# Kernel optimization log

Hardware: AMD Instinct MI355X
Metric: run time of the kernel (lower is better)

Reference implementation:

```python
import jax, jax.numpy as jnp
import numpy as np

S = 4096
DMODEL = 1024
DK = 128

def setup_inputs() -> dict:
    key = jax.random.key(0)
    ks = jax.random.split(key, 7)
    X = jax.random.normal(ks[0], (S, DMODEL), dtype=jnp.float32)
    # nn.Linear(dmodel, dk): weight [dk, dmodel], bias [dk]
    sc = 1.0 / np.sqrt(DMODEL)
    Wq = jax.random.uniform(ks[1], (DK, DMODEL), jnp.float32, -sc, sc)
    bq = jax.random.uniform(ks[2], (DK,), jnp.float32, -sc, sc)
    Wk = jax.random.uniform(ks[3], (DK, DMODEL), jnp.float32, -sc, sc)
    bk = jax.random.uniform(ks[4], (DK,), jnp.float32, -sc, sc)
    Wv = jax.random.uniform(ks[5], (DK, DMODEL), jnp.float32, -sc, sc)
    bv = jax.random.uniform(ks[6], (DK,), jnp.float32, -sc, sc)
    return {"X": X, "Wq": Wq, "bq": bq, "Wk": Wk, "bk": bk, "Wv": Wv, "bv": bv}

def reference(X, Wq, bq, Wk, bk, Wv, bv):
    # QKV projections: [S, dk]
    Q = X @ Wq.T + bq
    K = X @ Wk.T + bk
    V = X @ Wv.T + bv
    scale = 1.0 / jnp.sqrt(jnp.asarray(DK, X.dtype))
    scores = (Q @ K.T) * scale  # [S, S]
    s = X.shape[0]
    causal = jnp.tril(jnp.ones((s, s), dtype=bool))  # True = keep
    scores = jnp.where(causal, scores, -jnp.inf)
    A = jax.nn.softmax(scores, axis=-1)  # dropout p=0 -> identity
    return A @ V  # [S, dk]
```

## Files before the change

kernel.cpp:

```cpp
#include <hip/hip_runtime.h>
#include <hip/hip_bf16.h>

#define S 4096
#define DMODEL 1024
#define DK 128

typedef __attribute__((ext_vector_type(8))) short  short8;
typedef __attribute__((ext_vector_type(4))) float  f32x4;

__device__ __forceinline__ unsigned short f2bf(float f) {
    return __builtin_bit_cast(unsigned short, __float2bfloat16(f));
}

__device__ __forceinline__ short8 cvt8(float4 a, float4 b) {
    short8 v;
    v[0] = (short)f2bf(a.x); v[1] = (short)f2bf(a.y);
    v[2] = (short)f2bf(a.z); v[3] = (short)f2bf(a.w);
    v[4] = (short)f2bf(b.x); v[5] = (short)f2bf(b.y);
    v[6] = (short)f2bf(b.z); v[7] = (short)f2bf(b.w);
    return v;
}

__global__ __launch_bounds__(256) void cvt_kernel(
    const float* __restrict__ X,
    const float* __restrict__ Wq, const float* __restrict__ Wk,
    const float* __restrict__ Wv,
    unsigned short* __restrict__ Xb, unsigned short* __restrict__ Wb)
{
    const int i = blockIdx.x * 256 + threadIdx.x;
    const float* __restrict__ src;
    unsigned short* __restrict__ dst;
    size_t off;
    if (i < 524288) {
        src = X; dst = Xb; off = (size_t)i * 8;
    } else {
        const int j   = i - 524288;
        const int sel = j >> 14, jj = j & 16383;
        src = sel == 0 ? Wq : sel == 1 ? Wk : Wv;
        dst = Wb + (size_t)sel * DK * DMODEL;
        off = (size_t)jj * 8;
    }
    const float4 a = *(const float4*)(src + off);
    const float4 b = *(const float4*)(src + off + 4);
    *(short8*)(dst + off) = cvt8(a, b);
}

__global__ __launch_bounds__(256) void proj_gemm(
    const unsigned short* __restrict__ Xb, const unsigned short* __restrict__ Wb,
    const float* __restrict__ bq, const float* __restrict__ bk,
    const float* __restrict__ bv,
    unsigned short* __restrict__ Qb, unsigned short* __restrict__ Kb,
    unsigned short* __restrict__ Vb)
{
    const int sel = blockIdx.y;
    const float* __restrict__ bias = sel == 0 ? bq : sel == 1 ? bk : bv;
    unsigned short* __restrict__ Out = sel == 0 ? Qb : sel == 1 ? Kb : Vb;
    const unsigned short* __restrict__ wbase = Wb + (size_t)sel * DK * DMODEL;

    const int tid = threadIdx.x, w = tid >> 6, lane = tid & 63;
    const int li = lane & 15, gl = lane >> 4;
    const int r0 = blockIdx.x * 16;
    const int n0 = w * 32;

    f32x4 acc[2];
    #pragma unroll
    for (int j = 0; j < 2; ++j)
        #pragma unroll
        for (int r = 0; r < 4; ++r) acc[j][r] = 0.f;

    const unsigned short* ap = &Xb[(size_t)(r0 + li) * DMODEL + 8 * gl];
    const unsigned short* bp0 = &wbase[(size_t)(n0 + li) * DMODEL + 8 * gl];
    const unsigned short* bp1 = &wbase[(size_t)(n0 + 16 + li) * DMODEL + 8 * gl];

    #pragma unroll 4
    for (int k0 = 0; k0 < DMODEL; k0 += 32) {
        const short8 a  = *(const short8*)(ap + k0);
        const short8 b0 = *(const short8*)(bp0 + k0);
        const short8 b1 = *(const short8*)(bp1 + k0);
        acc[0] = __builtin_amdgcn_mfma_f32_16x16x32_bf16(a, b0, acc[0], 0, 0, 0);
        acc[1] = __builtin_amdgcn_mfma_f32_16x16x32_bf16(a, b1, acc[1], 0, 0, 0);
    }

    #pragma unroll
    for (int j = 0; j < 2; ++j)
        #pragma unroll
        for (int r = 0; r < 4; ++r) {
            const int row = r0 + 4 * gl + r;
            const int col = n0 + 16 * j + li;
            Out[(size_t)row * DK + col] = f2bf(acc[j][r] + bias[col]);
        }
}

__global__ __launch_bounds__(256) void transpose_v(
    const unsigned short* __restrict__ Vb, unsigned short* __restrict__ Vt)
{
    __shared__ unsigned short tile[64][72];
    const int s0 = blockIdx.x * 64, d0 = blockIdx.y * 64;
    const int t = threadIdx.x;
    const int r = t >> 2, cc = (t & 3) * 16;

    const short8* src = (const short8*)&Vb[(size_t)(s0 + r) * DK + d0 + cc];
    const short8 a = src[0], b = src[1];
    #pragma unroll
    for (int i = 0; i < 8; ++i) {
        tile[r][cc + i]     = (unsigned short)a[i];
        tile[r][cc + 8 + i] = (unsigned short)b[i];
    }
    __syncthreads();

    short8 o0, o1;
    #pragma unroll
    for (int i = 0; i < 8; ++i) {
        o0[i] = (short)tile[cc + i][r];
        o1[i] = (short)tile[cc + 8 + i][r];
    }
    short8* dst = (short8*)&Vt[(size_t)(d0 + r) * S + s0 + cc];
    dst[0] = o0; dst[1] = o1;
}

__global__ __launch_bounds__(64) void attn_mfma(
    const unsigned short* __restrict__ Qb,
    const unsigned short* __restrict__ Kb,
    const unsigned short* __restrict__ Vt,
    float* __restrict__ OP, float* __restrict__ ML)
{
    const int b = blockIdx.x;
    int g;
    if      (b <  32) g = 0; else if (b <  96) g = 1;
    else if (b < 192) g = 2; else if (b < 320) g = 3;
    else if (b < 480) g = 4; else if (b < 672) g = 5;
    else if (b < 896) g = 6; else               g = 7;
    const int off = b - 16 * g * (g + 1);
    const int qt  = 32 * g + off / (g + 1);
    const int c   = off % (g + 1);
    const int kstart = c * 512;
    const int kend   = min((c + 1) * 512, 16 * qt + 16);

    const int lane = threadIdx.x, li = lane & 15, gl = lane >> 4;
    const int qrow = 16 * qt + li;

    __shared__ unsigned short Pl[16][40];

    short8 aq[4];
    #pragma unroll
    for (int s = 0; s < 4; ++s)
        aq[s] = *(const short8*)&Qb[(size_t)qrow * DK + 32 * s + 8 * gl];

    f32x4 accv[8];
    #pragma unroll
    for (int n = 0; n < 8; ++n)
        #pragma unroll
        for (int r = 0; r < 4; ++r) accv[n][r] = 0.f;

    float mrow[4] = {-1e30f, -1e30f, -1e30f, -1e30f};
    float lrow[4] = {0.f, 0.f, 0.f, 0.f};
    const float scale = 0.08838834764831845f;

    for (int kb = kstart; kb < kend; kb += 32) {
        short8 bk[2][4], bv[8];
        #pragma unroll
        for (int kt = 0; kt < 2; ++kt)
            #pragma unroll
            for (int s = 0; s < 4; ++s)
                bk[kt][s] = *(const short8*)
                    &Kb[(size_t)(kb + 16 * kt + li) * DK + 32 * s + 8 * gl];
        #pragma unroll
        for (int n = 0; n < 8; ++n)
            bv[n] = *(const short8*)&Vt[(size_t)(16 * n + li) * S + kb + 8 * gl];

        f32x4 sc[2];
        #pragma unroll
        for (int kt = 0; kt < 2; ++kt)
            #pragma unroll
            for (int r = 0; r < 4; ++r) sc[kt][r] = 0.f;
        #pragma unroll
        for (int kt = 0; kt < 2; ++kt)
            #pragma unroll
            for (int s = 0; s < 4; ++s)
                sc[kt] = __builtin_amdgcn_mfma_f32_16x16x32_bf16(
                    aq[s], bk[kt][s], sc[kt], 0, 0, 0);

        float p[2][4];
        #pragma unroll
        for (int kt = 0; kt < 2; ++kt)
            #pragma unroll
            for (int r = 0; r < 4; ++r) {
                const int key = kb + 16 * kt + li;
                const int q   = 16 * qt + 4 * gl + r;
                p[kt][r] = (key > q) ? -1e30f : sc[kt][r] * scale;
            }

        #pragma unroll
        for (int r = 0; r < 4; ++r) {
            float t = fmaxf(p[0][r], p[1][r]);
            t = fmaxf(t, __shfl_xor(t, 1));
            t = fmaxf(t, __shfl_xor(t, 2));
            t = fmaxf(t, __shfl_xor(t, 4));
            t = fmaxf(t, __shfl_xor(t, 8));
            const float mnew = fmaxf(mrow[r], t);
            const float corr = __expf(mrow[r] - mnew);
            p[0][r] = __expf(p[0][r] - mnew);
            p[1][r] = __expf(p[1][r] - mnew);
            float ps = p[0][r] + p[1][r];
            ps += __shfl_xor(ps, 1);
            ps += __shfl_xor(ps, 2);
            ps += __shfl_xor(ps, 4);
            ps += __shfl_xor(ps, 8);
            lrow[r] = lrow[r] * corr + ps;
            mrow[r] = mnew;
            #pragma unroll
            for (int n = 0; n < 8; ++n) accv[n][r] *= corr;
        }

        #pragma unroll
        for (int kt = 0; kt < 2; ++kt)
            #pragma unroll
            for (int r = 0; r < 4; ++r)
                Pl[4 * gl + r][16 * kt + li] = f2bf(p[kt][r]);
        __syncthreads();
        const short8 pa = *(const short8*)&Pl[li][8 * gl];
        __syncthreads();

        #pragma unroll
        for (int n = 0; n < 8; ++n)
            accv[n] = __builtin_amdgcn_mfma_f32_16x16x32_bf16(pa, bv[n], accv[n], 0, 0, 0);
    }

    #pragma unroll
    for (int n = 0; n < 8; ++n)
        #pragma unroll
        for (int r = 0; r < 4; ++r)
            OP[((size_t)b * 16 + 4 * gl + r) * DK + 16 * n + li] = accv[n][r];
    if (li == 0) {
        #pragma unroll
        for (int r = 0; r < 4; ++r) {
            ML[((size_t)b * 16 + 4 * gl + r) * 2 + 0] = mrow[r];
            ML[((size_t)b * 16 + 4 * gl + r) * 2 + 1] = lrow[r];
        }
    }
}

__global__ __launch_bounds__(DK) void merge_kernel(
    const float* __restrict__ OP, const float* __restrict__ ML,
    float* __restrict__ out)
{
    const int row = blockIdx.x, dv = threadIdx.x;
    const int qt = row >> 4, ql = row & 15;
    const int g  = qt >> 5;
    const int base = 16 * g * (g + 1) + (qt & 31) * (g + 1);

    float M = -1e30f;
    for (int c = 0; c <= g; ++c)
        M = fmaxf(M, ML[((size_t)(base + c) * 16 + ql) * 2]);
    float L = 0.f, o = 0.f;
    for (int c = 0; c <= g; ++c) {
        const float mc = ML[((size_t)(base + c) * 16 + ql) * 2 + 0];
        const float lc = ML[((size_t)(base + c) * 16 + ql) * 2 + 1];
        const float wgt = __expf(mc - M);
        L += lc * wgt;
        o += wgt * OP[((size_t)(base + c) * 16 + ql) * DK + dv];
    }
    out[(size_t)row * DK + dv] = o / L;
}

extern "C" void kernel_launch(void* const* d_in, const int* in_sizes, int n_in,
                              void* d_out, int out_size, void* d_ws, size_t ws_size,
                              hipStream_t stream)
{
    (void)in_sizes; (void)n_in; (void)out_size; (void)ws_size;
    const float* X  = (const float*)d_in[0];
    const float* Wq = (const float*)d_in[1];
    const float* bq = (const float*)d_in[2];
    const float* Wk = (const float*)d_in[3];
    const float* bk = (const float*)d_in[4];
    const float* Wv = (const float*)d_in[5];
    const float* bv = (const float*)d_in[6];
    float* out = (float*)d_out;

    unsigned short* Wb = (unsigned short*)d_ws;
    unsigned short* Qb = Wb + (size_t)3 * DK * DMODEL;
    unsigned short* Kb = Qb + (size_t)S * DK;
    unsigned short* Vb = Kb + (size_t)S * DK;
    unsigned short* Vt = Vb + (size_t)S * DK;
    unsigned short* Xb = Vt + (size_t)S * DK;
    float* OP = (float*)Xb;
    float* ML = OP + (size_t)1152 * 16 * DK;

    cvt_kernel<<<2240, 256, 0, stream>>>(X, Wq, Wk, Wv, Xb, Wb);
    proj_gemm<<<dim3(S / 16, 3), 256, 0, stream>>>(
        Xb, Wb, bq, bk, bv, Qb, Kb, Vb);
    transpose_v<<<dim3(S / 64, DK / 64), 256, 0, stream>>>(Vb, Vt);
    attn_mfma<<<1152, 64, 0, stream>>>(Qb, Kb, Vt, OP, ML);
    merge_kernel<<<S, DK, 0, stream>>>(OP, ML, out);
}
```

Baseline: 159.6 us.

## Enlarge attention query tile to 32 rows, prefetch K, add lazy rescale

The attention kernel now processes 32 query rows per wavefront, sharing each loaded K/V tile across two 16-row subtiles. It also uses 256-key chunks with a new split schedule of 1088 blocks, software-prefetches the next K tile, and skips the online-softmax rescale unless the running max grows by more than a threshold. MFMA sections are bracketed with s_setprio. The projection GEMM uses 2 waves each computing 64 output columns instead of 4 waves of 32, so each A fragment is reused across more MFMAs. The cost is more registers per wave and fewer blocks, with some risk of lower occupancy. The lazy rescale leans on exp values staying bounded when the max shifts by less than the threshold.

```diff
diff --git a/kernel.cpp b/kernel.cpp
--- a/kernel.cpp
+++ b/kernel.cpp
@@ -45,7 +45,7 @@
     *(short8*)(dst + off) = cvt8(a, b);
 }
 
-__global__ __launch_bounds__(256) void proj_gemm(
+__global__ __launch_bounds__(128) void proj_gemm(
     const unsigned short* __restrict__ Xb, const unsigned short* __restrict__ Wb,
     const float* __restrict__ bq, const float* __restrict__ bk,
     const float* __restrict__ bv,
@@ -60,29 +60,35 @@
     const int tid = threadIdx.x, w = tid >> 6, lane = tid & 63;
     const int li = lane & 15, gl = lane >> 4;
     const int r0 = blockIdx.x * 16;
-    const int n0 = w * 32;
-
-    f32x4 acc[2];
-    #pragma unroll
-    for (int j = 0; j < 2; ++j)
+    const int n0 = w * 64;
+
+    f32x4 acc[4];
+    #pragma unroll
+    for (int j = 0; j < 4; ++j)
         #pragma unroll
         for (int r = 0; r < 4; ++r) acc[j][r] = 0.f;
 
     const unsigned short* ap = &Xb[(size_t)(r0 + li) * DMODEL + 8 * gl];
     const unsigned short* bp0 = &wbase[(size_t)(n0 + li) * DMODEL + 8 * gl];
-    const unsigned short* bp1 = &wbase[(size_t)(n0 + 16 + li) * DMODEL + 8 * gl];
+    const unsigned short* bp1 = bp0 + (size_t)16 * DMODEL;
+    const unsigned short* bp2 = bp0 + (size_t)32 * DMODEL;
+    const unsigned short* bp3 = bp0 + (size_t)48 * DMODEL;
 
     #pragma unroll 4
     for (int k0 = 0; k0 < DMODEL; k0 += 32) {
         const short8 a  = *(const short8*)(ap + k0);
         const short8 b0 = *(const short8*)(bp0 + k0);
         const short8 b1 = *(const short8*)(bp1 + k0);
+        const short8 b2 = *(const short8*)(bp2 + k0);
+        const short8 b3 = *(const short8*)(bp3 + k0);
         acc[0] = __builtin_amdgcn_mfma_f32_16x16x32_bf16(a, b0, acc[0], 0, 0, 0);
         acc[1] = __builtin_amdgcn_mfma_f32_16x16x32_bf16(a, b1, acc[1], 0, 0, 0);
-    }
-
-    #pragma unroll
-    for (int j = 0; j < 2; ++j)
+        acc[2] = __builtin_amdgcn_mfma_f32_16x16x32_bf16(a, b2, acc[2], 0, 0, 0);
+        acc[3] = __builtin_amdgcn_mfma_f32_16x16x32_bf16(a, b3, acc[3], 0, 0, 0);
+    }
+
+    #pragma unroll
+    for (int j = 0; j < 4; ++j)
         #pragma unroll
         for (int r = 0; r < 4; ++r) {
             const int row = r0 + 4 * gl + r;
@@ -125,118 +131,183 @@
     float* __restrict__ OP, float* __restrict__ ML)
 {
     const int b = blockIdx.x;
-    int g;
-    if      (b <  32) g = 0; else if (b <  96) g = 1;
-    else if (b < 192) g = 2; else if (b < 320) g = 3;
-    else if (b < 480) g = 4; else if (b < 672) g = 5;
-    else if (b < 896) g = 6; else               g = 7;
-    const int off = b - 16 * g * (g + 1);
-    const int qt  = 32 * g + off / (g + 1);
+    int g = 0;
+    while (4 * (g + 1) * (g + 2) <= b) ++g;
+    const int off = b - 4 * g * (g + 1);
+    const int t   = 8 * g + off / (g + 1);
     const int c   = off % (g + 1);
-    const int kstart = c * 512;
-    const int kend   = min((c + 1) * 512, 16 * qt + 16);
+    const int kstart = c * 256;
+    const int kend   = min((c + 1) * 256, 32 * t + 32);
 
     const int lane = threadIdx.x, li = lane & 15, gl = lane >> 4;
-    const int qrow = 16 * qt + li;
-
-    __shared__ unsigned short Pl[16][40];
-
-    short8 aq[4];
-    #pragma unroll
-    for (int s = 0; s < 4; ++s)
-        aq[s] = *(const short8*)&Qb[(size_t)qrow * DK + 32 * s + 8 * gl];
-
-    f32x4 accv[8];
-    #pragma unroll
-    for (int n = 0; n < 8; ++n)
-        #pragma unroll
-        for (int r = 0; r < 4; ++r) accv[n][r] = 0.f;
-
-    float mrow[4] = {-1e30f, -1e30f, -1e30f, -1e30f};
-    float lrow[4] = {0.f, 0.f, 0.f, 0.f};
+
+    __shared__ unsigned short Pl[32][40];
+
+    short8 aq[2][4];
+    #pragma unroll
+    for (int qs = 0; qs < 2; ++qs)
+        #pragma unroll
+        for (int s = 0; s < 4; ++s)
+            aq[qs][s] = *(const short8*)
+                &Qb[(size_t)(32 * t + 16 * qs + li) * DK + 32 * s + 8 * gl];
+
+    f32x4 accv[2][8];
+    #pragma unroll
+    for (int qs = 0; qs < 2; ++qs)
+        #pragma unroll
+        for (int n = 0; n < 8; ++n)
+            #pragma unroll
+            for (int r = 0; r < 4; ++r) accv[qs][n][r] = 0.f;
+
+    float mrow[2][4], lrow[2][4];
+    #pragma unroll
+    for (int qs = 0; qs < 2; ++qs)
+        #pragma unroll
+        for (int r = 0; r < 4; ++r) { mrow[qs][r] = -1e30f; lrow[qs][r] = 0.f; }
+
     const float scale = 0.08838834764831845f;
 
+    short8 bkc[2][4], bkn[2][4];
+    #pragma unroll
+    for (int kt = 0; kt < 2; ++kt)
+        #pragma unroll
+        for (int s = 0; s < 4; ++s)
+            bkc[kt][s] = *(const short8*)
+                &Kb[(size_t)(kstart + 16 * kt + li) * DK + 32 * s + 8 * gl];
+
     for (int kb = kstart; kb < kend; kb += 32) {
-        short8 bk[2][4], bv[8];
-        #pragma unroll
-        for (int kt = 0; kt < 2; ++kt)
-            #pragma unroll
-            for (int s = 0; s < 4; ++s)
-                bk[kt][s] = *(const short8*)
-                    &Kb[(size_t)(kb + 16 * kt + li) * DK + 32 * s + 8 * gl];
+        short8 bv[8];
         #pragma unroll
         for (int n = 0; n < 8; ++n)
             bv[n] = *(const short8*)&Vt[(size_t)(16 * n + li) * S + kb + 8 * gl];
 
-        f32x4 sc[2];
+        f32x4 sc[2][2];
+        #pragma unroll
+        for (int qs = 0; qs < 2; ++qs)
+            #pragma unroll
+            for (int kt = 0; kt < 2; ++kt)
+                #pragma unroll
+                for (int r = 0; r < 4; ++r) sc[qs][kt][r] = 0.f;
+        __builtin_amdgcn_s_setprio(1);
+        #pragma unroll
+        for (int qs = 0; qs < 2; ++qs)
+            #pragma unroll
+            for (int kt = 0; kt < 2; ++kt)
+                #pragma unroll
+                for (int s = 0; s < 4; ++s)
+                    sc[qs][kt] = __builtin_amdgcn_mfma_f32_16x16x32_bf16(
+                        aq[qs][s], bkc[kt][s], sc[qs][kt], 0, 0, 0);
+        __builtin_amdgcn_s_setprio(0);
+
+        const int kn = (kb + 32 < kend) ? kb + 32 : kb;
         #pragma unroll
         for (int kt = 0; kt < 2; ++kt)
             #pragma unroll
-            for (int r = 0; r < 4; ++r) sc[kt][r] = 0.f;
+            for (int s = 0; s < 4; ++s)
+                bkn[kt][s] = *(const short8*)
+                    &Kb[(size_t)(kn + 16 * kt + li) * DK + 32 * s + 8 * gl];
+
+        #pragma unroll
+        for (int qs = 0; qs < 2; ++qs)
+            #pragma unroll
+            for (int kt = 0; kt < 2; ++kt)
+                #pragma unroll
+                for (int r = 0; r < 4; ++r) {
+                    const int key = kb + 16 * kt + li;
+                    const int q   = 32 * t + 16 * qs + 4 * gl + r;
+                    sc[qs][kt][r] = (key > q) ? -1e30f : sc[qs][kt][r] * scale;
+                }
+
+        float tm[2][4];
+        #pragma unroll
+        for (int qs = 0; qs < 2; ++qs)
+            #pragma unroll
+            for (int r = 0; r < 4; ++r) {
+                float v = fmaxf(sc[qs][0][r], sc[qs][1][r]);
+                v = fmaxf(v, __shfl_xor(v, 1));
+                v = fmaxf(v, __shfl_xor(v, 2));
+                v = fmaxf(v, __shfl_xor(v, 4));
+                v = fmaxf(v, __shfl_xor(v, 8));
+                tm[qs][r] = v;
+            }
+
+        int need = 0;
+        #pragma unroll
+        for (int qs = 0; qs < 2; ++qs)
+            #pragma unroll
+            for (int r = 0; r < 4; ++r)
+                need |= (tm[qs][r] > mrow[qs][r] + 6.f) ? 1 : 0;
+        if (__any(need)) {
+            #pragma unroll
+            for (int qs = 0; qs < 2; ++qs)
+                #pragma unroll
+                for (int r = 0; r < 4; ++r) {
+                    const float mnew = fmaxf(mrow[qs][r], tm[qs][r]);
+                    const float corr = __expf(mrow[qs][r] - mnew);
+                    lrow[qs][r] *= corr;
+                    mrow[qs][r] = mnew;
+                    #pragma unroll
+                    for (int n = 0; n < 8; ++n) accv[qs][n][r] *= corr;
+                }
+        }
+
+        #pragma unroll
+        for (int qs = 0; qs < 2; ++qs)
+            #pragma unroll
+            for (int r = 0; r < 4; ++r) {
+                const float p0 = __expf(sc[qs][0][r] - mrow[qs][r]);
+                const float p1 = __expf(sc[qs][1][r] - mrow[qs][r]);
+                sc[qs][0][r] = p0; sc[qs][1][r] = p1;
+                float ps = p0 + p1;
+                ps += __shfl_xor(ps, 1);
+                ps += __shfl_xor(ps, 2);
+                ps += __shfl_xor(ps, 4);
+                ps += __shfl_xor(ps, 8);
+                lrow[qs][r] += ps;
+            }
+
+        #pragma unroll
+        for (int qs = 0; qs < 2; ++qs)
+            #pragma unroll
+            for (int kt = 0; kt < 2; ++kt)
+                #pragma unroll
+                for (int r = 0; r < 4; ++r)
+                    Pl[16 * qs + 4 * gl + r][16 * kt + li] = f2bf(sc[qs][kt][r]);
+        __syncthreads();
+        const short8 pa0 = *(const short8*)&Pl[li][8 * gl];
+        const short8 pa1 = *(const short8*)&Pl[16 + li][8 * gl];
+        __syncthreads();
+
+        __builtin_amdgcn_s_setprio(1);
+        #pragma unroll
+        for (int n = 0; n < 8; ++n) {
+            accv[0][n] = __builtin_amdgcn_mfma_f32_16x16x32_bf16(pa0, bv[n], accv[0][n], 0, 0, 0);
+            accv[1][n] = __builtin_amdgcn_mfma_f32_16x16x32_bf16(pa1, bv[n], accv[1][n], 0, 0, 0);
+        }
+        __builtin_amdgcn_s_setprio(0);
+
         #pragma unroll
         for (int kt = 0; kt < 2; ++kt)
             #pragma unroll
-            for (int s = 0; s < 4; ++s)
-                sc[kt] = __builtin_amdgcn_mfma_f32_16x16x32_bf16(
-                    aq[s], bk[kt][s], sc[kt], 0, 0, 0);
-
-        float p[2][4];
-        #pragma unroll
-        for (int kt = 0; kt < 2; ++kt)
+            for (int s = 0; s < 4; ++s) bkc[kt][s] = bkn[kt][s];
+    }
+
+    #pragma unroll
+    for (int qs = 0; qs < 2; ++qs)
+        #pragma unroll
+        for (int n = 0; n < 8; ++n)
+            #pragma unroll
+            for (int r = 0; r < 4; ++r)
+                OP[((size_t)b * 32 + 16 * qs + 4 * gl + r) * DK + 16 * n + li]
+                    = accv[qs][n][r];
+    if (li == 0) {
+        #pragma unroll
+        for (int qs = 0; qs < 2; ++qs)
             #pragma unroll
             for (int r = 0; r < 4; ++r) {
-                const int key = kb + 16 * kt + li;
-                const int q   = 16 * qt + 4 * gl + r;
-                p[kt][r] = (key > q) ? -1e30f : sc[kt][r] * scale;
+                ML[((size_t)b * 32 + 16 * qs + 4 * gl + r) * 2 + 0] = mrow[qs][r];
+                ML[((size_t)b * 32 + 16 * qs + 4 * gl + r) * 2 + 1] = lrow[qs][r];
             }
-
-        #pragma unroll
-        for (int r = 0; r < 4; ++r) {
-            float t = fmaxf(p[0][r], p[1][r]);
-            t = fmaxf(t, __shfl_xor(t, 1));
-            t = fmaxf(t, __shfl_xor(t, 2));
-            t = fmaxf(t, __shfl_xor(t, 4));
-            t = fmaxf(t, __shfl_xor(t, 8));
-            const float mnew = fmaxf(mrow[r], t);
-            const float corr = __expf(mrow[r] - mnew);
-            p[0][r] = __expf(p[0][r] - mnew);
-            p[1][r] = __expf(p[1][r] - mnew);
-            float ps = p[0][r] + p[1][r];
-            ps += __shfl_xor(ps, 1);
-            ps += __shfl_xor(ps, 2);
-            ps += __shfl_xor(ps, 4);
-            ps += __shfl_xor(ps, 8);
-            lrow[r] = lrow[r] * corr + ps;
-            mrow[r] = mnew;
-            #pragma unroll
-            for (int n = 0; n < 8; ++n) accv[n][r] *= corr;
-        }
-
-        #pragma unroll
-        for (int kt = 0; kt < 2; ++kt)
-            #pragma unroll
-            for (int r = 0; r < 4; ++r)
-                Pl[4 * gl + r][16 * kt + li] = f2bf(p[kt][r]);
-        __syncthreads();
-        const short8 pa = *(const short8*)&Pl[li][8 * gl];
-        __syncthreads();
-
-        #pragma unroll
-        for (int n = 0; n < 8; ++n)
-            accv[n] = __builtin_amdgcn_mfma_f32_16x16x32_bf16(pa, bv[n], accv[n], 0, 0, 0);
-    }
-
-    #pragma unroll
-    for (int n = 0; n < 8; ++n)
-        #pragma unroll
-        for (int r = 0; r < 4; ++r)
-            OP[((size_t)b * 16 + 4 * gl + r) * DK + 16 * n + li] = accv[n][r];
-    if (li == 0) {
-        #pragma unroll
-        for (int r = 0; r < 4; ++r) {
-            ML[((size_t)b * 16 + 4 * gl + r) * 2 + 0] = mrow[r];
-            ML[((size_t)b * 16 + 4 * gl + r) * 2 + 1] = lrow[r];
-        }
     }
 }
 
@@ -245,20 +316,20 @@
     float* __restrict__ out)
 {
     const int row = blockIdx.x, dv = threadIdx.x;
-    const int qt = row >> 4, ql = row & 15;
-    const int g  = qt >> 5;
-    const int base = 16 * g * (g + 1) + (qt & 31) * (g + 1);
+    const int t  = row >> 5, rl = row & 31;
+    const int g  = t >> 3;
+    const int base = 4 * g * (g + 1) + (t & 7) * (g + 1);
 
     float M = -1e30f;
     for (int c = 0; c <= g; ++c)
-        M = fmaxf(M, ML[((size_t)(base + c) * 16 + ql) * 2]);
+        M = fmaxf(M, ML[((size_t)(base + c) * 32 + rl) * 2]);
     float L = 0.f, o = 0.f;
     for (int c = 0; c <= g; ++c) {
-        const float mc = ML[((size_t)(base + c) * 16 + ql) * 2 + 0];
-        const float lc = ML[((size_t)(base + c) * 16 + ql) * 2 + 1];
+        const float mc = ML[((size_t)(base + c) * 32 + rl) * 2 + 0];
+        const float lc = ML[((size_t)(base + c) * 32 + rl) * 2 + 1];
         const float wgt = __expf(mc - M);
         L += lc * wgt;
-        o += wgt * OP[((size_t)(base + c) * 16 + ql) * DK + dv];
+        o += wgt * OP[((size_t)(base + c) * 32 + rl) * DK + dv];
     }
     out[(size_t)row * DK + dv] = o / L;
 }
@@ -284,12 +355,12 @@
     unsigned short* Vt = Vb + (size_t)S * DK;
     unsigned short* Xb = Vt + (size_t)S * DK;
     float* OP = (float*)Xb;
-    float* ML = OP + (size_t)1152 * 16 * DK;
+    float* ML = OP + (size_t)1088 * 32 * DK;
 
     cvt_kernel<<<2240, 256, 0, stream>>>(X, Wq, Wk, Wv, Xb, Wb);
-    proj_gemm<<<dim3(S / 16, 3), 256, 0, stream>>>(
+    proj_gemm<<<dim3(S / 16, 3), 128, 0, stream>>>(
         Xb, Wb, bq, bk, bv, Qb, Kb, Vb);
     transpose_v<<<dim3(S / 64, DK / 64), 256, 0, stream>>>(Vb, Vt);
-    attn_mfma<<<1152, 64, 0, stream>>>(Qb, Kb, Vt, OP, ML);
+    attn_mfma<<<1088, 64, 0, stream>>>(Qb, Kb, Vt, OP, ML);
     merge_kernel<<<S, DK, 0, stream>>>(OP, ML, out);
 }
```

Result: faster. 149.9 us (-6.1%).
